# Optimization experiments

Measured on AMD Instinct MI355X. Metric: run time of the kernel, lower is better.

## Reference

```python
import jax, jax.numpy as jnp
import numpy as np

D = 1024      # input_dim == attention_dim == num_heads*head_dim
H = 16        # num_heads
HD = 64       # head_dim
FF = 4096     # ff_dim
EPS = 1e-5


def _layernorm(x, gamma, beta):
    mu = jnp.mean(x, axis=-1, keepdims=True)
    var = jnp.var(x, axis=-1, keepdims=True)
    return (x - mu) * jax.lax.rsqrt(var + EPS) * gamma + beta


def setup_inputs() -> dict:
    key = jax.random.key(0)
    ks = jax.random.split(key, 11)
    s_in = 1.0 / np.sqrt(D)
    s_ff = 1.0 / np.sqrt(FF)
    return {
        "x": jax.random.normal(ks[0], (2, 2048, D), dtype=jnp.float32),
        "w_qkv": jax.random.uniform(ks[1], (D, 3 * D), jnp.float32, -s_in, s_in),
        "b_qkv": jax.random.uniform(ks[2], (3 * D,), jnp.float32, -s_in, s_in),
        "w_o": jax.random.uniform(ks[3], (D, D), jnp.float32, -s_in, s_in),
        "b_o": jax.random.uniform(ks[4], (D,), jnp.float32, -s_in, s_in),
        "g1": jnp.ones((D,), jnp.float32),
        "be1": jnp.zeros((D,), jnp.float32),
        "w1": jax.random.uniform(ks[5], (D, FF), jnp.float32, -s_in, s_in),
        "b1": jax.random.uniform(ks[6], (FF,), jnp.float32, -s_in, s_in),
        "w2": jax.random.uniform(ks[7], (FF, D), jnp.float32, -s_ff, s_ff),
        "b2": jax.random.uniform(ks[8], (D,), jnp.float32, -s_ff, s_ff),
        "g2": jnp.ones((D,), jnp.float32),
        "be2": jnp.zeros((D,), jnp.float32),
    }


def reference(x, w_qkv, b_qkv, w_o, b_o, g1, be1, w1, b1, w2, b2, g2, be2):
    N, L, _ = x.shape
    qkv = x @ w_qkv + b_qkv                       # [N, L, 3D]
    q = qkv[..., :D].reshape(N, L, H, HD)
    k = qkv[..., D:2 * D].reshape(N, L, H, HD)
    v = qkv[..., 2 * D:].reshape(N, L, H, HD)
    scores = jnp.einsum('nqhd,nkhd->nhqk', q, k) / np.sqrt(HD)
    attn = jax.nn.softmax(scores, axis=-1)        # [N, H, L, L]
    out = jnp.einsum('nhql,nlhd->nqhd', attn, v).reshape(N, L, D)
    attn_out = out @ w_o + b_o
    # dropout is identity in eval mode
    h = _layernorm(attn_out + x, g1, be1)
    ff = jax.nn.relu(h @ w1 + b1) @ w2 + b2
    return _layernorm(h + ff, g2, be2)
```

## Files before the change

kernel.cpp:

```cpp
#include <hip/hip_runtime.h>
#include <cstddef>
#include <cstdint>

static constexpr int Dm   = 1024;
static constexpr int Hh   = 16;
static constexpr int HDd  = 64;
static constexpr int FFd  = 4096;
static constexpr int Ls   = 2048;
static constexpr int Nb   = 2;
static constexpr int Mrows = Nb * Ls;

typedef short bf16x8 __attribute__((ext_vector_type(8)));
typedef float f32x4  __attribute__((ext_vector_type(4)));

#if __has_builtin(__builtin_amdgcn_exp2f)
#define EXP2(x) __builtin_amdgcn_exp2f(x)
#else
#define EXP2(x) exp2f(x)
#endif

__device__ __forceinline__ ushort f2b(float f) {
    uint32_t u = __builtin_bit_cast(uint32_t, f);
    u = (u + 0x7FFFu + ((u >> 16) & 1u)) >> 16;
    return (ushort)u;
}
__device__ __forceinline__ ushort f2bf(float f) {
    return (ushort)((__builtin_bit_cast(uint32_t, f) + 0x8000u) >> 16);
}
__device__ __forceinline__ float b2f(ushort b) {
    return __builtin_bit_cast(float, (uint32_t)b << 16);
}

__device__ __forceinline__ void gl2lds16(const ushort* g, ushort* l) {
    __builtin_amdgcn_global_load_lds(
        (const __attribute__((address_space(1))) void*)g,
        (__attribute__((address_space(3))) void*)l, 16, 0, 0);
}

template <int RELU>
__device__ __forceinline__ void pack_store_pair(
    ushort* __restrict__ C, int N, int m0, int n, int lane,
    const f32x4 a, float bv)
{
    float v0 = a[0] + bv, v1 = a[1] + bv, v2 = a[2] + bv, v3 = a[3] + bv;
    if (RELU) {
        v0 = fmaxf(v0, 0.f); v1 = fmaxf(v1, 0.f);
        v2 = fmaxf(v2, 0.f); v3 = fmaxf(v3, 0.f);
    }
    uint32_t a01 = (uint32_t)f2bf(v0) | ((uint32_t)f2bf(v1) << 16);
    uint32_t a23 = (uint32_t)f2bf(v2) | ((uint32_t)f2bf(v3) << 16);
    uint32_t x01 = (uint32_t)__shfl_xor((int)a01, 1);
    uint32_t x23 = (uint32_t)__shfl_xor((int)a23, 1);
    const bool ev = (lane & 1) == 0;
    const uint32_t low  = ev ? a01 : x23;
    const uint32_t high = ev ? x01 : a23;
    const uint32_t dA = (low & 0xFFFFu) | (high << 16);
    const uint32_t dB = (low >> 16) | (high & 0xFFFF0000u);
    const int rb = ev ? 0 : 2;
    const int nc = n - (lane & 1);
    *(uint32_t*)(C + (size_t)(m0 + rb) * N + nc)     = dA;
    *(uint32_t*)(C + (size_t)(m0 + rb + 1) * N + nc) = dB;
}

__global__ __launch_bounds__(256) void prep(
    const float* __restrict__ x, ushort* __restrict__ xb,
    const float* __restrict__ w_qkv, ushort* __restrict__ wqkvT,
    const float* __restrict__ w_o, ushort* __restrict__ woT,
    const float* __restrict__ w1, ushort* __restrict__ w1T,
    const float* __restrict__ w2, ushort* __restrict__ w2T)
{
    __shared__ float t[32][33];
    const int bid = blockIdx.x;
    const int tidx = threadIdx.x;
    if (bid < 4096) {
        const int i = bid * 1024 + tidx * 4;
        float4 v = *(const float4*)(x + i);
        uint2 o;
        o.x = (uint32_t)f2b(v.x) | ((uint32_t)f2b(v.y) << 16);
        o.y = (uint32_t)f2b(v.z) | ((uint32_t)f2b(v.w) << 16);
        *(uint2*)(xb + i) = o;
        return;
    }
    const float* src; ushort* dst; int K, N, r;
    if (bid < 7168)       { r = bid - 4096;  src = w_qkv; dst = wqkvT; K = Dm;  N = 3 * Dm; }
    else if (bid < 8192)  { r = bid - 7168;  src = w_o;   dst = woT;   K = Dm;  N = Dm;  }
    else if (bid < 12288) { r = bid - 8192;  src = w1;    dst = w1T;   K = Dm;  N = FFd; }
    else                  { r = bid - 12288; src = w2;    dst = w2T;   K = FFd; N = Dm;  }
    const int gx = N / 32;
    const int bx = r % gx, by = r / gx;
    const int k0 = by * 32, n0 = bx * 32;
    const int tx = tidx & 31, ty = tidx >> 5;
    #pragma unroll
    for (int i = 0; i < 4; ++i)
        t[ty + i * 8][tx] = src[(size_t)(k0 + ty + i * 8) * N + n0 + tx];
    __syncthreads();
    #pragma unroll
    for (int i = 0; i < 4; ++i)
        dst[(size_t)(n0 + ty + i * 8) * K + k0 + tx] = f2b(t[tx][ty + i * 8]);
}

template <int TN, int RELU, int VOUT, int SPLITK>
__global__ __launch_bounds__(256) void gemm_mfma(
    const ushort* __restrict__ A, const ushort* __restrict__ Bt,
    const float* __restrict__ bias,
    ushort* __restrict__ Cb, ushort* __restrict__ vT, int M, int N, int K)
{
    constexpr int NT  = TN / 32;
    constexpr int BSZ = TN * 32;
    __shared__ __align__(16) ushort As[2 * 128 * 32];
    __shared__ __align__(16) ushort Bs[2 * BSZ];

    const int tid  = threadIdx.x;
    int bx, by;
    {
        const int gx = gridDim.x;
        const int nwg = gx * gridDim.y;
        const int lin = blockIdx.y * gx + blockIdx.x;
        const int swz = (lin & 7) * (nwg >> 3) + (lin >> 3);
        by = swz / gx; bx = swz - by * gx;
    }
    const int bm   = by * 128, bn = bx * TN;
    const int wave = tid >> 6, lane = tid & 63;
    const int wm = (wave & 1) * 64;
    const int wn = (wave >> 1) * (TN / 2);
    const int lr = lane & 15, lq = lane >> 4;

    const int KS   = K / SPLITK;
    const int Koff = (SPLITK > 1) ? blockIdx.z * KS : 0;

    const int rr = wave * 16 + (lane >> 2);
    const int sg = lane & 3;
    const ushort* Ag = A  + (size_t)(bm + rr) * K + Koff + sg * 8;
    const ushort* Bg = Bt + (size_t)(bn + rr) * K + Koff + sg * 8;

    f32x4 acc[4][NT];
    #pragma unroll
    for (int i = 0; i < 4; ++i)
        #pragma unroll
        for (int j = 0; j < NT; ++j)
            acc[i][j] = (f32x4){0.f, 0.f, 0.f, 0.f};

    gl2lds16(Ag,                  As + wave * 512);
    gl2lds16(Ag + (size_t)64 * K, As + 2048 + wave * 512);
    gl2lds16(Bg,                  Bs + wave * 512);
    if (TN == 128)
        gl2lds16(Bg + (size_t)64 * K, Bs + 2048 + wave * 512);
    if (TN == 96) {
        if (wave < 2)
            gl2lds16(Bg + (size_t)64 * K, Bs + 2048 + wave * 512);
    }

    int ib = 0;
    for (int k0 = 0; k0 < KS; k0 += 32, ib ^= 1) {
        __syncthreads();
        if (k0 + 32 < KS) {
            const int nb = ib ^ 1;
            gl2lds16(Ag + k0 + 32,                  As + nb * 4096 + wave * 512);
            gl2lds16(Ag + k0 + 32 + (size_t)64 * K, As + nb * 4096 + 2048 + wave * 512);
            gl2lds16(Bg + k0 + 32,                  Bs + nb * BSZ + wave * 512);
            if (TN == 128)
                gl2lds16(Bg + k0 + 32 + (size_t)64 * K, Bs + nb * BSZ + 2048 + wave * 512);
            if (TN == 96) {
                if (wave < 2)
                    gl2lds16(Bg + k0 + 32 + (size_t)64 * K, Bs + nb * BSZ + 2048 + wave * 512);
            }
        }

        const ushort* Ar = As + ib * 4096;
        const ushort* Br = Bs + ib * BSZ;
        bf16x8 af[4], bf[NT];
        #pragma unroll
        for (int mt = 0; mt < 4; ++mt)
            af[mt] = *(const bf16x8*)(Ar + (wm + mt * 16 + lr) * 32 + lq * 8);
        #pragma unroll
        for (int nt = 0; nt < NT; ++nt)
            bf[nt] = *(const bf16x8*)(Br + (wn + nt * 16 + lr) * 32 + lq * 8);

        #pragma unroll
        for (int mt = 0; mt < 4; ++mt)
            #pragma unroll
            for (int nt = 0; nt < NT; ++nt)
                acc[mt][nt] = __builtin_amdgcn_mfma_f32_16x16x32_bf16(
                    af[mt], bf[nt], acc[mt][nt], 0, 0, 0);
    }

    if (SPLITK > 1) {
        ushort* Cp = Cb + (size_t)blockIdx.z * M * N;
        #pragma unroll
        for (int nt = 0; nt < NT; ++nt) {
            const int n = bn + wn + nt * 16 + lr;
            #pragma unroll
            for (int mt = 0; mt < 4; ++mt)
                pack_store_pair<0>(Cp, N, bm + wm + mt * 16 + lq * 4, n, lane,
                                   acc[mt][nt], 0.0f);
        }
        return;
    }
    if (VOUT) {
        const int batch = bm >> 11;
        #pragma unroll
        for (int nt = 0; nt < NT; ++nt) {
            const int n = bn + wn + nt * 16 + lr;
            const float bv = bias[n];
            if (bn + wn + nt * 16 >= 2 * Dm) {
                const int col = n - 2 * Dm;
                const int h = col >> 6, d = col & 63;
                uint2 p4[4];
                #pragma unroll
                for (int mt = 0; mt < 4; ++mt) {
                    p4[mt].x = (uint32_t)f2bf(acc[mt][nt][0] + bv) |
                               ((uint32_t)f2bf(acc[mt][nt][1] + bv) << 16);
                    p4[mt].y = (uint32_t)f2bf(acc[mt][nt][2] + bv) |
                               ((uint32_t)f2bf(acc[mt][nt][3] + bv) << 16);
                }
                uint2 q4[4];
                #pragma unroll
                for (int mt = 0; mt < 4; ++mt) {
                    q4[mt].x = (uint32_t)__shfl_xor((int)p4[mt].x, 16);
                    q4[mt].y = (uint32_t)__shfl_xor((int)p4[mt].y, 16);
                }
                ushort* drow = vT + (((size_t)(batch * Hh + h)) * HDd + d) * Ls;
                const bool evq = (lq & 1) == 0;
                #pragma unroll
                for (int t = 0; t < 2; ++t) {
                    const int mt = (evq ? 0 : 2) + t;
                    const int key = (bm + wm + mt * 16 + (lq & ~1) * 4) & (Ls - 1);
                    uint4 w;
                    if (evq) w = (uint4){p4[mt].x, p4[mt].y, q4[mt].x, q4[mt].y};
                    else     w = (uint4){q4[mt].x, q4[mt].y, p4[mt].x, p4[mt].y};
                    *(uint4*)(drow + key) = w;
                }
            } else {
                #pragma unroll
                for (int mt = 0; mt < 4; ++mt)
                    pack_store_pair<0>(Cb, N, bm + wm + mt * 16 + lq * 4, n, lane,
                                       acc[mt][nt], bv);
            }
        }
        return;
    }
    #pragma unroll
    for (int nt = 0; nt < NT; ++nt) {
        const int n = bn + wn + nt * 16 + lr;
        const float bv = bias[n];
        #pragma unroll
        for (int mt = 0; mt < 4; ++mt)
            pack_store_pair<RELU>(Cb, N, bm + wm + mt * 16 + lq * 4, n, lane,
                                  acc[mt][nt], bv);
    }
}

__global__ __launch_bounds__(256) void attn_mfma(
    const ushort* __restrict__ qkv, const ushort* __restrict__ vT,
    float* __restrict__ npart, float* __restrict__ dpart)
{
    const int tid = threadIdx.x, wave = tid >> 6, lane = tid & 63;
    const int lr = lane & 15, lq = lane >> 4;
    int bx, h, z;
    {
        const int lin = (blockIdx.z * 16 + blockIdx.y) * 16 + blockIdx.x;
        const int swz = (lin & 7) * 128 + (lin >> 3);
        bx = swz & 15; h = (swz >> 4) & 15; z = swz >> 8;
    }
    const int n = z >> 1, kv = z & 1;
    const int kt0 = kv * (Ls / 2);
    const int q0 = bx * 128 + wave * 32;
    const size_t RS = 3 * Dm;
    const ushort* base  = qkv + (size_t)n * Ls * RS;
    const ushort* vbase = vT + (size_t)(n * Hh + h) * HDd * Ls;

    __shared__ __align__(16) ushort Kb[64 * 72];
    __shared__ __align__(16) ushort Vt[64 * 72];

    bf16x8 qf[2][2];
    {
        const float c = 0.18033688011112042f;
        #pragma unroll
        for (int qh = 0; qh < 2; ++qh) {
            const ushort* qg = base + (size_t)(q0 + qh * 16 + lr) * RS + h * HDd + lq * 8;
            bf16x8 t0 = *(const bf16x8*)(qg);
            bf16x8 t1 = *(const bf16x8*)(qg + 32);
            #pragma unroll
            for (int j = 0; j < 8; ++j) {
                qf[0][qh][j] = (short)f2b(b2f((ushort)t0[j]) * c);
                qf[1][qh][j] = (short)f2b(b2f((ushort)t1[j]) * c);
            }
        }
    }

    bf16x8 onesf;
    #pragma unroll
    for (int j = 0; j < 8; ++j) onesf[j] = (short)0x3F80;
    const f32x4 z4 = (f32x4){0.f, 0.f, 0.f, 0.f};

    f32x4 o[4][2];
    #pragma unroll
    for (int dt = 0; dt < 4; ++dt)
        #pragma unroll
        for (int qh = 0; qh < 2; ++qh)
            o[dt][qh] = (f32x4){0.f, 0.f, 0.f, 0.f};
    f32x4 dacc[2];
    dacc[0] = (f32x4){0.f, 0.f, 0.f, 0.f};
    dacc[1] = (f32x4){0.f, 0.f, 0.f, 0.f};

    const int srow = tid >> 2, ssg = tid & 3;
    const ushort* kg = base + (size_t)srow * RS + Dm + h * HDd;
    const ushort* vg = vbase + (size_t)srow * Ls;

    const int sA = (((2 * ssg) & 3) * 8) + (((ssg >> 1) & 1) * 4);
    const int sB = (((2 * ssg + 1) & 3) * 8) + (((ssg >> 1) & 1) * 4);

    int4 ka = *(const int4*)(kg + (size_t)kt0 * RS + ssg * 8);
    int4 kb = *(const int4*)(kg + (size_t)kt0 * RS + (ssg + 4) * 8);
    int4 va = *(const int4*)(vg + kt0 + ssg * 8);
    int4 vb = *(const int4*)(vg + kt0 + (ssg + 4) * 8);

    for (int kt = kt0; kt < kt0 + Ls / 2; kt += 64) {
        __syncthreads();
        *(int4*)(Kb + srow * 72 + ssg * 8)       = ka;
        *(int4*)(Kb + srow * 72 + (ssg + 4) * 8) = kb;
        {
            ushort* vrow = Vt + srow * 72;
            *(uint2*)(vrow + sA)      = (uint2){(uint32_t)va.x, (uint32_t)va.y};
            *(uint2*)(vrow + sB)      = (uint2){(uint32_t)va.z, (uint32_t)va.w};
            *(uint2*)(vrow + 32 + sA) = (uint2){(uint32_t)vb.x, (uint32_t)vb.y};
            *(uint2*)(vrow + 32 + sB) = (uint2){(uint32_t)vb.z, (uint32_t)vb.w};
        }
        __syncthreads();

        if (kt + 64 < kt0 + Ls / 2) {
            const ushort* kp = kg + (size_t)(kt + 64) * RS;
            const ushort* vp = vg + (kt + 64);
            ka = *(const int4*)(kp + ssg * 8);
            kb = *(const int4*)(kp + (ssg + 4) * 8);
            va = *(const int4*)(vp + ssg * 8);
            vb = *(const int4*)(vp + (ssg + 4) * 8);
        }

        f32x4 s[4][2];
        #pragma unroll
        for (int ks = 0; ks < 2; ++ks)
            #pragma unroll
            for (int mt = 0; mt < 4; ++mt) {
                bf16x8 kf = *(const bf16x8*)(Kb + (mt * 16 + lr) * 72 + ks * 32 + lq * 8);
                #pragma unroll
                for (int qh = 0; qh < 2; ++qh)
                    s[mt][qh] = __builtin_amdgcn_mfma_f32_16x16x32_bf16(
                        kf, qf[ks][qh], ks == 0 ? z4 : s[mt][qh], 0, 0, 0);
            }

        uint2 pb[4][2];
        #pragma unroll
        for (int mt = 0; mt < 4; ++mt)
            #pragma unroll
            for (int qh = 0; qh < 2; ++qh) {
                float p0 = EXP2(s[mt][qh][0]);
                float p1 = EXP2(s[mt][qh][1]);
                float p2 = EXP2(s[mt][qh][2]);
                float p3 = EXP2(s[mt][qh][3]);
                uint32_t w0, w1;
                asm("v_cvt_pk_bf16_f32 %0, %1, %2" : "=v"(w0) : "v"(p0), "v"(p1));
                asm("v_cvt_pk_bf16_f32 %0, %1, %2" : "=v"(w1) : "v"(p2), "v"(p3));
                pb[mt][qh].x = w0;
                pb[mt][qh].y = w1;
            }

        #pragma unroll
        for (int ks = 0; ks < 2; ++ks) {
            bf16x8 pf[2];
            #pragma unroll
            for (int qh = 0; qh < 2; ++qh) {
                uint4 u = (uint4){pb[2 * ks][qh].x, pb[2 * ks][qh].y,
                                  pb[2 * ks + 1][qh].x, pb[2 * ks + 1][qh].y};
                pf[qh] = __builtin_bit_cast(bf16x8, u);
            }
            #pragma unroll
            for (int dt = 0; dt < 4; ++dt) {
                bf16x8 vf = *(const bf16x8*)(Vt + (dt * 16 + lr) * 72 + ks * 32 + lq * 8);
                #pragma unroll
                for (int qh = 0; qh < 2; ++qh)
                    o[dt][qh] = __builtin_amdgcn_mfma_f32_16x16x32_bf16(
                        vf, pf[qh], o[dt][qh], 0, 0, 0);
            }
            #pragma unroll
            for (int qh = 0; qh < 2; ++qh)
                dacc[qh] = __builtin_amdgcn_mfma_f32_16x16x32_bf16(
                    onesf, pf[qh], dacc[qh], 0, 0, 0);
        }
    }

    const int idx = kv * Nb + n;
    #pragma unroll
    for (int qh = 0; qh < 2; ++qh) {
        float* nrow = npart + ((size_t)idx * Ls + q0 + qh * 16 + lr) * Dm + h * HDd;
        #pragma unroll
        for (int dt = 0; dt < 4; ++dt) {
            float4 o4 = {o[dt][qh][0], o[dt][qh][1], o[dt][qh][2], o[dt][qh][3]};
            *(float4*)(nrow + dt * 16 + lq * 4) = o4;
        }
        if (lane < 16)
            dpart[((size_t)idx * Hh + h) * Ls + q0 + qh * 16 + lane] = dacc[qh][0];
    }
}

__global__ __launch_bounds__(256) void attn_combine(
    const float* __restrict__ npart, const float* __restrict__ dpart,
    ushort* __restrict__ out)
{
    const int row = blockIdx.x;
    const int tid = threadIdx.x;
    const int n = row >> 11, q = row & (Ls - 1);
    const int h = tid >> 4;

    const size_t b0 = ((size_t)(0 * Nb + n) * Ls + q) * Dm;
    const size_t b1 = ((size_t)(1 * Nb + n) * Ls + q) * Dm;
    float4 a = ((const float4*)(npart + b0))[tid];
    float4 b = ((const float4*)(npart + b1))[tid];
    const float d0 = dpart[((size_t)(0 * Nb + n) * Hh + h) * Ls + q];
    const float d1 = dpart[((size_t)(1 * Nb + n) * Hh + h) * Ls + q];
    const float inv = 1.0f / (d0 + d1);

    ushort4 ob;
    ob.x = f2bf((a.x + b.x) * inv);
    ob.y = f2bf((a.y + b.y) * inv);
    ob.z = f2bf((a.z + b.z) * inv);
    ob.w = f2bf((a.w + b.w) * inv);
    *(ushort4*)(out + (size_t)row * Dm + tid * 4) = ob;
}

template <int NP, int OTHER_BF16, int OUT_F32>
__global__ __launch_bounds__(256) void addn_ln(
    const ushort* __restrict__ part, const void* __restrict__ other,
    const float* __restrict__ bias,
    const float* __restrict__ gamma, const float* __restrict__ beta,
    float* __restrict__ outf, ushort* __restrict__ outb)
{
    const int row = blockIdx.x;
    const int tid = threadIdx.x;

    float4 bv = ((const float4*)bias)[tid];
    float v[4];
    if (OTHER_BF16) {
        ushort4 u = ((const ushort4*)((const ushort*)other + (size_t)row * Dm))[tid];
        v[0] = b2f(u.x) + bv.x; v[1] = b2f(u.y) + bv.y;
        v[2] = b2f(u.z) + bv.z; v[3] = b2f(u.w) + bv.w;
    } else {
        float4 f = ((const float4*)((const float*)other + (size_t)row * Dm))[tid];
        v[0] = f.x + bv.x; v[1] = f.y + bv.y; v[2] = f.z + bv.z; v[3] = f.w + bv.w;
    }
    #pragma unroll
    for (int pp = 0; pp < NP; ++pp) {
        ushort4 u = ((const ushort4*)(part + (size_t)pp * Mrows * Dm
                                           + (size_t)row * Dm))[tid];
        v[0] += b2f(u.x); v[1] += b2f(u.y); v[2] += b2f(u.z); v[3] += b2f(u.w);
    }

    float s  = v[0] + v[1] + v[2] + v[3];
    float sq = v[0]*v[0] + v[1]*v[1] + v[2]*v[2] + v[3]*v[3];

    __shared__ float red[8];
    #pragma unroll
    for (int off = 32; off > 0; off >>= 1) {
        s  += __shfl_down(s, off);
        sq += __shfl_down(sq, off);
    }
    const int wv = tid >> 6;
    if ((tid & 63) == 0) { red[wv] = s; red[4 + wv] = sq; }
    __syncthreads();
    s  = red[0] + red[1] + red[2] + red[3];
    sq = red[4] + red[5] + red[6] + red[7];

    const float mu  = s * (1.0f / Dm);
    const float var = sq * (1.0f / Dm) - mu * mu;
    const float inv = rsqrtf(var + 1e-5f);

    const float4 g  = ((const float4*)gamma)[tid];
    const float4 be = ((const float4*)beta)[tid];
    float ov[4];
    ov[0] = (v[0] - mu) * inv * g.x + be.x;
    ov[1] = (v[1] - mu) * inv * g.y + be.y;
    ov[2] = (v[2] - mu) * inv * g.z + be.z;
    ov[3] = (v[3] - mu) * inv * g.w + be.w;
    if (OUT_F32) {
        float4 o4 = {ov[0], ov[1], ov[2], ov[3]};
        ((float4*)(outf + (size_t)row * Dm))[tid] = o4;
    } else {
        uint2 ob;
        ob.x = (uint32_t)f2bf(ov[0]) | ((uint32_t)f2bf(ov[1]) << 16);
        ob.y = (uint32_t)f2bf(ov[2]) | ((uint32_t)f2bf(ov[3]) << 16);
        *(uint2*)(outb + (size_t)row * Dm + tid * 4) = ob;
    }
}

extern "C" void kernel_launch(void* const* d_in, const int* in_sizes, int n_in,
                              void* d_out, int out_size, void* d_ws, size_t ws_size,
                              hipStream_t stream)
{
    const float* x     = (const float*)d_in[0];
    const float* w_qkv = (const float*)d_in[1];
    const float* b_qkv = (const float*)d_in[2];
    const float* w_o   = (const float*)d_in[3];
    const float* b_o   = (const float*)d_in[4];
    const float* g1    = (const float*)d_in[5];
    const float* be1   = (const float*)d_in[6];
    const float* w1    = (const float*)d_in[7];
    const float* b1    = (const float*)d_in[8];
    const float* w2    = (const float*)d_in[9];
    const float* b2    = (const float*)d_in[10];
    const float* g2    = (const float*)d_in[11];
    const float* be2   = (const float*)d_in[12];
    float* out = (float*)d_out;

    char* p = (char*)d_ws;
    ushort* part4 = (ushort*)p;  p += (size_t)4 * Mrows * Dm * 2;
    ushort* qkvb  = (ushort*)p;  p += (size_t)Mrows * 3 * Dm * 2;
    ushort* hb    = (ushort*)p;  p += (size_t)Mrows * Dm * 2;
    ushort* ffb   = (ushort*)p;  p += (size_t)Mrows * FFd * 2;
    ushort* wqkvT = (ushort*)p;  p += (size_t)(3 * Dm) * Dm * 2;
    ushort* woT   = (ushort*)p;  p += (size_t)Dm * Dm * 2;
    ushort* w1T   = (ushort*)p;  p += (size_t)FFd * Dm * 2;
    ushort* w2T   = (ushort*)p;  p += (size_t)Dm * FFd * 2;
    ushort* vTg   = (ushort*)p;  p += (size_t)Mrows * Dm * 2;

    ushort* attnb = part4 + (size_t)2 * Mrows * Dm;
    ushort* xb    = part4 + (size_t)3 * Mrows * Dm;
    float* npart = (float*)ffb;
    float* dpart = (float*)part4;

    prep<<<dim3(16384), dim3(256), 0, stream>>>(
        x, xb, w_qkv, wqkvT, w_o, woT, w1, w1T, w2, w2T);

    gemm_mfma<96, 0, 1, 1><<<dim3(3 * Dm / 96, Mrows / 128), dim3(256), 0, stream>>>(
        xb, wqkvT, b_qkv, qkvb, vTg, Mrows, 3 * Dm, Dm);

    attn_mfma<<<dim3(Ls / 128, Hh, 2 * Nb), dim3(256), 0, stream>>>(qkvb, vTg, npart, dpart);
    attn_combine<<<dim3(Mrows), dim3(256), 0, stream>>>(npart, dpart, attnb);

    gemm_mfma<64, 0, 0, 2><<<dim3(Dm / 64, Mrows / 128, 2), dim3(256), 0, stream>>>(
        attnb, woT, nullptr, part4, nullptr, Mrows, Dm, Dm);

    addn_ln<2, 0, 0><<<dim3(Mrows), dim3(256), 0, stream>>>(
        part4, x, b_o, g1, be1, nullptr, hb);

    gemm_mfma<128, 1, 0, 1><<<dim3(FFd / 128, Mrows / 128), dim3(256), 0, stream>>>(
        hb, w1T, b1, ffb, nullptr, Mrows, FFd, Dm);

    gemm_mfma<128, 0, 0, 4><<<dim3(Dm / 128, Mrows / 128, 4), dim3(256), 0, stream>>>(
        ffb, w2T, nullptr, part4, nullptr, Mrows, Dm, FFd);

    addn_ln<4, 1, 1><<<dim3(Mrows), dim3(256), 0, stream>>>(
        part4, hb, b2, g2, be2, out, nullptr);
}
```

Before: 368.9 us.

## Fuse split-KV attention combine into attention kernel via in-block LDS reduction

```diff
diff --git a/kernel.cpp b/kernel.cpp
--- a/kernel.cpp
+++ b/kernel.cpp
@@ -250,27 +250,29 @@
     }
 }
 
-__global__ __launch_bounds__(256) void attn_mfma(
+__global__ __launch_bounds__(512) void attn_mfma(
     const ushort* __restrict__ qkv, const ushort* __restrict__ vT,
-    float* __restrict__ npart, float* __restrict__ dpart)
+    ushort* __restrict__ out)
 {
     const int tid = threadIdx.x, wave = tid >> 6, lane = tid & 63;
+    const int g = wave >> 2, wv = wave & 3;
     const int lr = lane & 15, lq = lane >> 4;
-    int bx, h, z;
+    int bx, h, n;
     {
         const int lin = (blockIdx.z * 16 + blockIdx.y) * 16 + blockIdx.x;
-        const int swz = (lin & 7) * 128 + (lin >> 3);
-        bx = swz & 15; h = (swz >> 4) & 15; z = swz >> 8;
-    }
-    const int n = z >> 1, kv = z & 1;
-    const int kt0 = kv * (Ls / 2);
-    const int q0 = bx * 128 + wave * 32;
+        const int swz = (lin & 7) * 64 + (lin >> 3);
+        bx = swz & 15; h = (swz >> 4) & 15; n = swz >> 8;
+    }
+    const int q0 = bx * 128 + wv * 32;
+    const int kt0 = g * (Ls / 2);
     const size_t RS = 3 * Dm;
     const ushort* base  = qkv + (size_t)n * Ls * RS;
     const ushort* vbase = vT + (size_t)(n * Hh + h) * HDd * Ls;
 
-    __shared__ __align__(16) ushort Kb[64 * 72];
-    __shared__ __align__(16) ushort Vt[64 * 72];
+    __shared__ __align__(16) ushort KV[4][64 * 72];
+    __shared__ __align__(16) float cmb[34][256];
+    ushort* Kb = KV[2 * g];
+    ushort* Vt = KV[2 * g + 1];
 
     bf16x8 qf[2][2];
     {
@@ -303,7 +305,8 @@
     dacc[0] = (f32x4){0.f, 0.f, 0.f, 0.f};
     dacc[1] = (f32x4){0.f, 0.f, 0.f, 0.f};
 
-    const int srow = tid >> 2, ssg = tid & 3;
+    const int lt = tid & 255;
+    const int srow = lt >> 2, ssg = lt & 3;
     const ushort* kg = base + (size_t)srow * RS + Dm + h * HDd;
     const ushort* vg = vbase + (size_t)srow * Ls;
 
@@ -389,43 +392,44 @@
         }
     }
 
-    const int idx = kv * Nb + n;
-    #pragma unroll
-    for (int qh = 0; qh < 2; ++qh) {
-        float* nrow = npart + ((size_t)idx * Ls + q0 + qh * 16 + lr) * Dm + h * HDd;
-        #pragma unroll
-        for (int dt = 0; dt < 4; ++dt) {
-            float4 o4 = {o[dt][qh][0], o[dt][qh][1], o[dt][qh][2], o[dt][qh][3]};
-            *(float4*)(nrow + dt * 16 + lq * 4) = o4;
-        }
-        if (lane < 16)
-            dpart[((size_t)idx * Hh + h) * Ls + q0 + qh * 16 + lane] = dacc[qh][0];
-    }
-}
-
-__global__ __launch_bounds__(256) void attn_combine(
-    const float* __restrict__ npart, const float* __restrict__ dpart,
-    ushort* __restrict__ out)
-{
-    const int row = blockIdx.x;
-    const int tid = threadIdx.x;
-    const int n = row >> 11, q = row & (Ls - 1);
-    const int h = tid >> 4;
-
-    const size_t b0 = ((size_t)(0 * Nb + n) * Ls + q) * Dm;
-    const size_t b1 = ((size_t)(1 * Nb + n) * Ls + q) * Dm;
-    float4 a = ((const float4*)(npart + b0))[tid];
-    float4 b = ((const float4*)(npart + b1))[tid];
-    const float d0 = dpart[((size_t)(0 * Nb + n) * Hh + h) * Ls + q];
-    const float d1 = dpart[((size_t)(1 * Nb + n) * Hh + h) * Ls + q];
-    const float inv = 1.0f / (d0 + d1);
-
-    ushort4 ob;
-    ob.x = f2bf((a.x + b.x) * inv);
-    ob.y = f2bf((a.y + b.y) * inv);
-    ob.z = f2bf((a.z + b.z) * inv);
-    ob.w = f2bf((a.w + b.w) * inv);
-    *(ushort4*)(out + (size_t)row * Dm + tid * 4) = ob;
+    const int c = wv * 64 + lane;
+    __syncthreads();
+    if (g == 1) {
+        #pragma unroll
+        for (int dt = 0; dt < 4; ++dt)
+            #pragma unroll
+            for (int qh = 0; qh < 2; ++qh)
+                #pragma unroll
+                for (int r = 0; r < 4; ++r)
+                    cmb[dt * 8 + qh * 4 + r][c] = o[dt][qh][r];
+        cmb[32][c] = dacc[0][0];
+        cmb[33][c] = dacc[1][0];
+    }
+    __syncthreads();
+    if (g == 0) {
+        #pragma unroll
+        for (int dt = 0; dt < 4; ++dt)
+            #pragma unroll
+            for (int qh = 0; qh < 2; ++qh)
+                #pragma unroll
+                for (int r = 0; r < 4; ++r)
+                    o[dt][qh][r] += cmb[dt * 8 + qh * 4 + r][c];
+        const float d0 = dacc[0][0] + cmb[32][c];
+        const float d1 = dacc[1][0] + cmb[33][c];
+        #pragma unroll
+        for (int qh = 0; qh < 2; ++qh) {
+            const float inv = 1.0f / (qh == 0 ? d0 : d1);
+            ushort* orow = out + (size_t)(n * Ls + q0 + qh * 16 + lr) * Dm + h * HDd;
+            #pragma unroll
+            for (int dt = 0; dt < 4; ++dt) {
+                ushort4 ob;
+                ushort* op = (ushort*)&ob;
+                #pragma unroll
+                for (int r = 0; r < 4; ++r) op[r] = f2bf(o[dt][qh][r] * inv);
+                *(ushort4*)(orow + dt * 16 + lq * 4) = ob;
+            }
+        }
+    }
 }
 
 template <int NP, int OTHER_BF16, int OUT_F32>
@@ -524,8 +528,6 @@
 
     ushort* attnb = part4 + (size_t)2 * Mrows * Dm;
     ushort* xb    = part4 + (size_t)3 * Mrows * Dm;
-    float* npart = (float*)ffb;
-    float* dpart = (float*)part4;
 
     prep<<<dim3(16384), dim3(256), 0, stream>>>(
         x, xb, w_qkv, wqkvT, w_o, woT, w1, w1T, w2, w2T);
@@ -533,8 +535,7 @@
     gemm_mfma<96, 0, 1, 1><<<dim3(3 * Dm / 96, Mrows / 128), dim3(256), 0, stream>>>(
         xb, wqkvT, b_qkv, qkvb, vTg, Mrows, 3 * Dm, Dm);
 
-    attn_mfma<<<dim3(Ls / 128, Hh, 2 * Nb), dim3(256), 0, stream>>>(qkvb, vTg, npart, dpart);
-    attn_combine<<<dim3(Mrows), dim3(256), 0, stream>>>(npart, dpart, attnb);
+    attn_mfma<<<dim3(Ls / 128, Hh, Nb), dim3(512), 0, stream>>>(qkvb, vTg, attnb);
 
     gemm_mfma<64, 0, 0, 2><<<dim3(Dm / 64, Mrows / 128, 2), dim3(256), 0, stream>>>(
         attnb, woT, nullptr, part4, nullptr, Mrows, Dm, Dm);
```

Result: faster. 359.5 us (-2.6%).
